# Kernel optimization log

Hardware: AMD Instinct MI355X
Metric: run time of the kernel (lower is better)

Reference implementation:

```python
import jax, jax.numpy as jnp
import numpy as np

H, M, K, V, FF = 16, 1024, 64, 64, 4096
B, C = 2, 2048
EPS = 1e-5


def layer_norm(x, g, b):
    mu = jnp.mean(x, axis=-1, keepdims=True)
    var = jnp.mean(jnp.square(x - mu), axis=-1, keepdims=True)
    return (x - mu) * jax.lax.rsqrt(var + EPS) * g + b


def setup_inputs() -> dict:
    key = jax.random.key(0)
    ks = jax.random.split(key, 7)
    return {
        "x": jax.random.normal(ks[0], (B, C, M), dtype=jnp.float32),
        "wq": jax.random.normal(ks[1], (H, M, K), dtype=jnp.float32),
        "wk": jax.random.normal(ks[2], (H, M, K), dtype=jnp.float32),
        "wv": jax.random.normal(ks[3], (H, M, V), dtype=jnp.float32),
        "wo": jax.random.normal(ks[4], (H, V, M), dtype=jnp.float32),
        "ln1_g": jnp.ones((M,), jnp.float32),
        "ln1_b": jnp.zeros((M,), jnp.float32),
        "w1": jax.random.normal(ks[5], (M, FF), dtype=jnp.float32),
        "b1": jnp.zeros((FF,), jnp.float32),
        "w2": jax.random.normal(ks[6], (FF, M), dtype=jnp.float32),
        "b2": jnp.zeros((M,), jnp.float32),
        "ln2_g": jnp.ones((M,), jnp.float32),
        "ln2_b": jnp.zeros((M,), jnp.float32),
    }


def reference(x, wq, wk, wv, wo, ln1_g, ln1_b, w1, b1, w2, b2, ln2_g, ln2_b):
    # --- multi-head self-attention (kv = q = x) ---
    kval = jnp.einsum('bcm,hmk->bhck', x, wk)
    vval = jnp.einsum('bcm,hmv->bhcv', x, wv)
    qval = jnp.einsum('bdm,hmk->bhdk', x, wq)
    # logits: c indexes keys, d indexes queries; softmax over keys (axis 2)
    logits = jnp.einsum('bhck,bhdk->bhcd', kval, qval) / np.sqrt(K).astype(np.float32)
    att = jax.nn.softmax(logits, axis=2)
    pre = jnp.einsum('bhcd,bhcv->bhdv', att, vval)
    attn_out = jnp.einsum('bhdv,hvm->bdm', pre, wo)
    h1 = layer_norm(x + attn_out, ln1_g, ln1_b)
    # --- position-wise FFN ---
    s = jax.nn.relu(jnp.einsum('bcm,mf->bcf', h1, w1) + b1)
    ffn_out = jnp.einsum('bcf,fm->bcm', s, w2) + b2
    return layer_norm(h1 + ffn_out, ln2_g, ln2_b)
```

## Files before the change

kernel.cpp:

```cpp
#include <hip/hip_runtime.h>
#include <hip/hip_bf16.h>

#define Hn 16
#define Mn 1024
#define FFn 4096
#define Bn 2
#define Cn 2048
#define EPSf 1e-5f
#define MB (1024LL*1024LL)

typedef unsigned short u16;
typedef __attribute__((ext_vector_type(8))) short bf16x8;
typedef __attribute__((ext_vector_type(4))) float f32x4;
typedef __attribute__((ext_vector_type(8))) unsigned short u16x8;

#define MFMA(a,b,c) __builtin_amdgcn_mfma_f32_16x16x32_bf16(a, b, c, 0, 0, 0)

__device__ __forceinline__ u16 f2b(float v) {
    union { float f; unsigned int u; } x; x.f = v;
    unsigned int r = x.u + 0x7fffu + ((x.u >> 16) & 1u);
    return (u16)(r >> 16);
}
__device__ __forceinline__ float b2f(u16 b) {
    union { unsigned int u; float f; } x; x.u = ((unsigned int)b) << 16;
    return x.f;
}
__device__ __forceinline__ void glds16(const void* g, void* l) {
    __builtin_amdgcn_global_load_lds((const __attribute__((address_space(1))) void*)g,
                                     (__attribute__((address_space(3))) void*)l, 16, 0, 0);
}

__global__ __launch_bounds__(256) void split_cvt(const float* __restrict__ in,
    u16* __restrict__ hi, u16* __restrict__ lo)
{
    const long i = ((long)blockIdx.x * 256 + threadIdx.x) * 8;
    float4 a = *(const float4*)&in[i];
    float4 b = *(const float4*)&in[i + 4];
    float v[8] = {a.x,a.y,a.z,a.w,b.x,b.y,b.z,b.w};
    u16x8 h, l;
#pragma unroll
    for (int j = 0; j < 8; ++j) {
        u16 hh = f2b(v[j]);
        h[j] = hh;
        l[j] = f2b(v[j] - b2f(hh));
    }
    *(u16x8*)&hi[i] = h;
    *(u16x8*)&lo[i] = l;
}

template<bool SPLIT>
__global__ __launch_bounds__(256) void tcvt(const float* __restrict__ in,
    u16* __restrict__ outh, u16* __restrict__ outl, int R, int Cc)
{
    __shared__ float ts[64][65];
    const int t = threadIdx.x;
    const long ib = (long)blockIdx.z * R * Cc;
    const int r0 = blockIdx.y * 64, c0 = blockIdx.x * 64;
    const int rr = t >> 2, cb = (t & 3) * 16;
#pragma unroll
    for (int u = 0; u < 4; ++u) {
        float4 v = *(const float4*)&in[ib + (long)(r0 + rr) * Cc + c0 + cb + u * 4];
        ts[rr][cb + u*4 + 0] = v.x; ts[rr][cb + u*4 + 1] = v.y;
        ts[rr][cb + u*4 + 2] = v.z; ts[rr][cb + u*4 + 3] = v.w;
    }
    __syncthreads();
    const int oc = t >> 2;
#pragma unroll
    for (int u = 0; u < 4; ++u) {
        float vv[4];
#pragma unroll
        for (int j = 0; j < 4; ++j) vv[j] = ts[cb + u*4 + j][oc];
        ushort4 hh;
        hh.x = f2b(vv[0]); hh.y = f2b(vv[1]); hh.z = f2b(vv[2]); hh.w = f2b(vv[3]);
        *(ushort4*)&outh[ib + (long)(c0 + oc) * R + r0 + cb + u*4] = hh;
        if (SPLIT) {
            ushort4 ll;
            ll.x = f2b(vv[0] - b2f(hh.x)); ll.y = f2b(vv[1] - b2f(hh.y));
            ll.z = f2b(vv[2] - b2f(hh.z)); ll.w = f2b(vv[3] - b2f(hh.w));
            *(ushort4*)&outl[ib + (long)(c0 + oc) * R + r0 + cb + u*4] = ll;
        }
    }
}

__global__ __launch_bounds__(256) void ttrans(const u16* __restrict__ in,
    u16* __restrict__ out, int R, int Cc)
{
    __shared__ u16 ts[64][72];
    const int t = threadIdx.x;
    const long ib = (long)blockIdx.z * R * Cc;
    const int r0 = blockIdx.y * 64, c0 = blockIdx.x * 64;
    const int rr = t >> 2, cb = (t & 3) * 16;
#pragma unroll
    for (int u = 0; u < 2; ++u)
        *(u16x8*)&ts[rr][cb + u*8] =
            *(const u16x8*)&in[ib + (long)(r0 + rr) * Cc + c0 + cb + u*8];
    __syncthreads();
    const int oc = t >> 2;
#pragma unroll
    for (int u = 0; u < 4; ++u) {
        ushort4 p;
        p.x = ts[cb + u*4 + 0][oc]; p.y = ts[cb + u*4 + 1][oc];
        p.z = ts[cb + u*4 + 2][oc]; p.w = ts[cb + u*4 + 3][oc];
        *(ushort4*)&out[ib + (long)(c0 + oc) * R + r0 + cb + u*4] = p;
    }
}

template<bool OUTB16, bool BIAS, bool RELU>
__global__ __launch_bounds__(256) void gemm128(
    const u16* __restrict__ A, const u16* __restrict__ Bt,
    const float* __restrict__ bias, void* __restrict__ Cout,
    int Kdim, int lda, int ldbt, int ldc)
{
    __shared__ u16 Als[128*32];
    __shared__ u16 Bls[128*32];
    const int t = threadIdx.x, w = t >> 6, l = t & 63;
    const int wm = w >> 1, wn = w & 1;
    const long row0 = (long)blockIdx.y * 128;
    const int n0 = blockIdx.x * 128;
    const int sr = l >> 2, sc = (l & 3) * 8;
    f32x4 acc[4][4] = {};
    for (int k0 = 0; k0 < Kdim; k0 += 32) {
        __syncthreads();
#pragma unroll
        for (int i = 0; i < 2; ++i) {
            const int c = w*2 + i;
            glds16(&A[(row0 + c*16 + sr) * lda + k0 + sc], (char*)Als + c*1024);
            glds16(&Bt[((long)n0 + c*16 + sr) * ldbt + k0 + sc], (char*)Bls + c*1024);
        }
        __syncthreads();
        bf16x8 af[4], bfv[4];
#pragma unroll
        for (int mf = 0; mf < 4; ++mf)
            af[mf] = *(const bf16x8*)&Als[(wm*64 + mf*16 + (l&15))*32 + (l>>4)*8];
#pragma unroll
        for (int nf = 0; nf < 4; ++nf)
            bfv[nf] = *(const bf16x8*)&Bls[(wn*64 + nf*16 + (l&15))*32 + (l>>4)*8];
#pragma unroll
        for (int mf = 0; mf < 4; ++mf)
#pragma unroll
            for (int nf = 0; nf < 4; ++nf)
                acc[mf][nf] = MFMA(af[mf], bfv[nf], acc[mf][nf]);
    }
#pragma unroll
    for (int nf = 0; nf < 4; ++nf) {
        const int col = n0 + wn*64 + nf*16 + (l & 15);
        const float bv = BIAS ? bias[col] : 0.f;
#pragma unroll
        for (int mf = 0; mf < 4; ++mf)
#pragma unroll
            for (int r = 0; r < 4; ++r) {
                const long row = row0 + wm*64 + mf*16 + (l>>4)*4 + r;
                float v = acc[mf][nf][r] + bv;
                if (RELU) v = fmaxf(v, 0.f);
                if (OUTB16) ((u16*)Cout)[row * ldc + col] = f2b(v);
                else        ((float*)Cout)[row * ldc + col] = v;
            }
    }
}

template<bool SIN, bool SOUT>
__global__ __launch_bounds__(256) void gemm64(
    const u16* __restrict__ Ah, const u16* __restrict__ Alo,
    const u16* __restrict__ Bth, const u16* __restrict__ Btl,
    u16* __restrict__ Chi, u16* __restrict__ Clo, float scale,
    int Kdim, int lda, int ldbt,
    int aDiv, long aStride, int bMod, long bStride, long cStride)
{
    extern __shared__ u16 lds[];
    u16* AH = lds;
    u16* BH = lds + 4096;
    u16* AL = lds + 6144;
    u16* BL = lds + 10240;
    const int t = threadIdx.x, w = t >> 6, l = t & 63;
    const int wm = w >> 1, wn = w & 1;
    const int z = blockIdx.z;
    const u16* Ahb = Ah + (long)(z / aDiv) * aStride;
    const u16* Alb = SIN ? (Alo + (long)(z / aDiv) * aStride) : (const u16*)nullptr;
    const u16* Bhb = Bth + (long)(z % bMod) * bStride;
    const u16* Blb = SIN ? (Btl + (long)(z % bMod) * bStride) : (const u16*)nullptr;
    const long row0 = (long)blockIdx.y * 128;
    const int sr = l >> 2, sc = (l & 3) * 8;
    f32x4 acc[4][2] = {};
    const int NCH = SIN ? 6 : 3;
    for (int k0 = 0; k0 < Kdim; k0 += 32) {
        __syncthreads();
        for (int i = 0; i < NCH; ++i) {
            const int idx = w + i*4;
            if (idx < 8)
                glds16(&Ahb[(row0 + idx*16 + sr)*lda + k0 + sc], (char*)AH + idx*1024);
            else if (idx < 12)
                glds16(&Bhb[(long)((idx-8)*16 + sr)*ldbt + k0 + sc], (char*)BH + (idx-8)*1024);
            else if (idx < 20)
                glds16(&Alb[(row0 + (idx-12)*16 + sr)*lda + k0 + sc], (char*)AL + (idx-12)*1024);
            else
                glds16(&Blb[(long)((idx-20)*16 + sr)*ldbt + k0 + sc], (char*)BL + (idx-20)*1024);
        }
        __syncthreads();
        bf16x8 ah[4], bh[2], al[4], bl[2];
#pragma unroll
        for (int mf = 0; mf < 4; ++mf)
            ah[mf] = *(const bf16x8*)&AH[(wm*64 + mf*16 + (l&15))*32 + (l>>4)*8];
#pragma unroll
        for (int nf = 0; nf < 2; ++nf)
            bh[nf] = *(const bf16x8*)&BH[(wn*32 + nf*16 + (l&15))*32 + (l>>4)*8];
        if (SIN) {
#pragma unroll
            for (int mf = 0; mf < 4; ++mf)
                al[mf] = *(const bf16x8*)&AL[(wm*64 + mf*16 + (l&15))*32 + (l>>4)*8];
#pragma unroll
            for (int nf = 0; nf < 2; ++nf)
                bl[nf] = *(const bf16x8*)&BL[(wn*32 + nf*16 + (l&15))*32 + (l>>4)*8];
        }
#pragma unroll
        for (int mf = 0; mf < 4; ++mf)
#pragma unroll
            for (int nf = 0; nf < 2; ++nf) {
                acc[mf][nf] = MFMA(ah[mf], bh[nf], acc[mf][nf]);
                if (SIN) {
                    acc[mf][nf] = MFMA(ah[mf], bl[nf], acc[mf][nf]);
                    acc[mf][nf] = MFMA(al[mf], bh[nf], acc[mf][nf]);
                }
            }
    }
    u16* Cb  = Chi + (long)z * cStride;
    u16* Clb = SOUT ? (Clo + (long)z * cStride) : (u16*)nullptr;
#pragma unroll
    for (int mf = 0; mf < 4; ++mf)
#pragma unroll
        for (int nf = 0; nf < 2; ++nf)
#pragma unroll
            for (int r = 0; r < 4; ++r) {
                const long row = row0 + wm*64 + mf*16 + (l>>4)*4 + r;
                const int col = wn*32 + nf*16 + (l & 15);
                const float v = acc[mf][nf][r] * scale;
                const u16 hh = f2b(v);
                Cb[row*64 + col] = hh;
                if (SOUT) Clb[row*64 + col] = f2b(v - b2f(hh));
            }
}

__global__ __launch_bounds__(256) void attn_mfma(
    const u16* __restrict__ qh, const u16* __restrict__ ql,
    const u16* __restrict__ kh, const u16* __restrict__ kl,
    const u16* __restrict__ vt, u16* __restrict__ pre2b)
{
    __shared__ u16 QH[4096], QL[4096], KH[4096], KL[4096], VT[4096];
    __shared__ u16 PL[4][1152];
    const int t = threadIdx.x, w = t >> 6, l = t & 63;
    const int bh = blockIdx.y, b = bh >> 4, h = bh & 15;
    const int q0 = blockIdx.x * 64;
    const long base = (long)bh * Cn * 64;
    const int srow = l >> 3;
    const int gch  = (l & 7) ^ (l >> 3);

#pragma unroll
    for (int i = 0; i < 2; ++i) {
        const int ci = w*2 + i;
        const int row = ci*8 + srow;
        glds16(&qh[base + (long)(q0 + row)*64 + gch*8], (char*)QH + ci*1024);
        glds16(&ql[base + (long)(q0 + row)*64 + gch*8], (char*)QL + ci*1024);
    }
    __syncthreads();
    bf16x8 qfh[2], qfl[2];
#pragma unroll
    for (int ks = 0; ks < 2; ++ks) {
        const int row = w*16 + (l & 15);
        const int ch = ((l>>4) + ks*4) ^ (row & 7);
        qfh[ks] = *(const bf16x8*)&QH[row*64 + ch*8];
        qfl[ks] = *(const bf16x8*)&QL[row*64 + ch*8];
    }
    float m_[4], ls_[4];
    f32x4 o[4] = {};
#pragma unroll
    for (int r = 0; r < 4; ++r) { m_[r] = -1e30f; ls_[r] = 0.f; }

    for (int c0 = 0; c0 < Cn; c0 += 64) {
        __syncthreads();
#pragma unroll
        for (int i = 0; i < 2; ++i) {
            const int ci = w*2 + i;
            const int row = ci*8 + srow;
            glds16(&kh[base + (long)(c0 + row)*64 + gch*8], (char*)KH + ci*1024);
            glds16(&kl[base + (long)(c0 + row)*64 + gch*8], (char*)KL + ci*1024);
            glds16(&vt[base + (long)row*Cn + c0 + gch*8],   (char*)VT + ci*1024);
        }
        __syncthreads();
        f32x4 sc[4];
#pragma unroll
        for (int cf = 0; cf < 4; ++cf) {
            f32x4 a = {0.f, 0.f, 0.f, 0.f};
#pragma unroll
            for (int ks = 0; ks < 2; ++ks) {
                const int row = cf*16 + (l & 15);
                const int ch = ((l>>4) + ks*4) ^ (row & 7);
                const bf16x8 kfh = *(const bf16x8*)&KH[row*64 + ch*8];
                const bf16x8 kfl = *(const bf16x8*)&KL[row*64 + ch*8];
                a = MFMA(qfh[ks], kfh, a);
                a = MFMA(qfh[ks], kfl, a);
                a = MFMA(qfl[ks], kfh, a);
            }
            sc[cf] = a;
        }
        float mx[4];
#pragma unroll
        for (int r = 0; r < 4; ++r)
            mx[r] = fmaxf(fmaxf(sc[0][r], sc[1][r]), fmaxf(sc[2][r], sc[3][r]));
#pragma unroll
        for (int off = 1; off < 16; off <<= 1)
#pragma unroll
            for (int r = 0; r < 4; ++r)
                mx[r] = fmaxf(mx[r], __shfl_xor(mx[r], off, 64));
        float fct[4], rs_[4];
#pragma unroll
        for (int r = 0; r < 4; ++r) {
            const float mn = fmaxf(m_[r], mx[r]);
            fct[r] = __expf(m_[r] - mn);
            m_[r] = mn;
            rs_[r] = 0.f;
        }
#pragma unroll
        for (int cf = 0; cf < 4; ++cf)
#pragma unroll
            for (int r = 0; r < 4; ++r) {
                const float p = __expf(sc[cf][r] - m_[r]);
                rs_[r] += p;
                PL[w][((l>>4)*4 + r)*72 + cf*16 + (l & 15)] = f2b(p);
            }
#pragma unroll
        for (int off = 1; off < 16; off <<= 1)
#pragma unroll
            for (int r = 0; r < 4; ++r)
                rs_[r] += __shfl_xor(rs_[r], off, 64);
#pragma unroll
        for (int r = 0; r < 4; ++r)
            ls_[r] = ls_[r] * fct[r] + rs_[r];
#pragma unroll
        for (int vf = 0; vf < 4; ++vf)
#pragma unroll
            for (int r = 0; r < 4; ++r)
                o[vf][r] *= fct[r];
        bf16x8 pa[2];
#pragma unroll
        for (int ks = 0; ks < 2; ++ks)
            pa[ks] = *(const bf16x8*)&PL[w][(l&15)*72 + ks*32 + (l>>4)*8];
#pragma unroll
        for (int vf = 0; vf < 4; ++vf)
#pragma unroll
            for (int ks = 0; ks < 2; ++ks) {
                const int row = vf*16 + (l & 15);
                const int ch = ((l>>4) + ks*4) ^ (row & 7);
                const bf16x8 vfr = *(const bf16x8*)&VT[row*64 + ch*8];
                o[vf] = MFMA(pa[ks], vfr, o[vf]);
            }
    }
    float inv[4];
#pragma unroll
    for (int r = 0; r < 4; ++r) inv[r] = 1.f / ls_[r];
#pragma unroll
    for (int vf = 0; vf < 4; ++vf)
#pragma unroll
        for (int r = 0; r < 4; ++r) {
            const long q = q0 + w*16 + (l>>4)*4 + r;
            pre2b[((long)b*Cn + q)*1024 + h*64 + vf*16 + (l&15)] = f2b(o[vf][r] * inv[r]);
        }
}

template<bool WB16>
__global__ __launch_bounds__(256) void ln_res(
    const float* __restrict__ a, const float* __restrict__ r,
    const float* __restrict__ g, const float* __restrict__ be,
    float* __restrict__ out, u16* __restrict__ outb)
{
    __shared__ float wsum[4];
    __shared__ float wsum2[4];
    const long row = blockIdx.x;
    const int t = threadIdx.x;
    float4 va = *(const float4*)&a[row * Mn + t * 4];
    float4 vb = *(const float4*)&r[row * Mn + t * 4];
    float v0 = va.x + vb.x, v1 = va.y + vb.y, v2 = va.z + vb.z, v3 = va.w + vb.w;

    float s = v0 + v1 + v2 + v3;
#pragma unroll
    for (int off = 32; off > 0; off >>= 1) s += __shfl_xor(s, off, 64);
    if ((t & 63) == 0) wsum[t >> 6] = s;
    __syncthreads();
    float mu = (wsum[0] + wsum[1] + wsum[2] + wsum[3]) * (1.0f / Mn);

    float d0 = v0 - mu, d1 = v1 - mu, d2 = v2 - mu, d3 = v3 - mu;
    float s2 = d0 * d0 + d1 * d1 + d2 * d2 + d3 * d3;
#pragma unroll
    for (int off = 32; off > 0; off >>= 1) s2 += __shfl_xor(s2, off, 64);
    if ((t & 63) == 0) wsum2[t >> 6] = s2;
    __syncthreads();
    float var = (wsum2[0] + wsum2[1] + wsum2[2] + wsum2[3]) * (1.0f / Mn);
    float rstd = rsqrtf(var + EPSf);

    float4 g4 = *(const float4*)&g[t * 4];
    float4 b4 = *(const float4*)&be[t * 4];
    float4 r4;
    r4.x = d0 * rstd * g4.x + b4.x;
    r4.y = d1 * rstd * g4.y + b4.y;
    r4.z = d2 * rstd * g4.z + b4.z;
    r4.w = d3 * rstd * g4.w + b4.w;
    *(float4*)&out[row * Mn + t * 4] = r4;
    if (WB16) {
        ushort4 ob;
        ob.x = f2b(r4.x); ob.y = f2b(r4.y); ob.z = f2b(r4.z); ob.w = f2b(r4.w);
        *(ushort4*)&outb[row * Mn + t * 4] = ob;
    }
}

extern "C" void kernel_launch(void* const* d_in, const int* in_sizes, int n_in,
                              void* d_out, int out_size, void* d_ws, size_t ws_size,
                              hipStream_t stream)
{
    const float* x    = (const float*)d_in[0];
    const float* wq   = (const float*)d_in[1];
    const float* wk   = (const float*)d_in[2];
    const float* wv   = (const float*)d_in[3];
    const float* wo   = (const float*)d_in[4];
    const float* ln1g = (const float*)d_in[5];
    const float* ln1b = (const float*)d_in[6];
    const float* w1   = (const float*)d_in[7];
    const float* b1   = (const float*)d_in[8];
    const float* w2   = (const float*)d_in[9];
    const float* b2   = (const float*)d_in[10];
    const float* ln2g = (const float*)d_in[11];
    const float* ln2b = (const float*)d_in[12];
    float* out = (float*)d_out;

    char* W = (char*)d_ws;
    u16* x_hi  = (u16*)(W + 0*MB);
    u16* x_lo  = (u16*)(W + 8*MB);
    u16* wqTh  = (u16*)(W + 16*MB);
    u16* wqTl  = (u16*)(W + 18*MB);
    u16* wkTh  = (u16*)(W + 20*MB);
    u16* wkTl  = (u16*)(W + 22*MB);
    u16* wvT   = (u16*)(W + 24*MB);
    u16* woT   = (u16*)(W + 26*MB);
    u16* q_hi  = (u16*)(W + 28*MB);
    u16* q_lo  = (u16*)(W + 36*MB);
    u16* k_hi  = (u16*)(W + 44*MB);
    u16* k_lo  = (u16*)(W + 52*MB);
    u16* vb    = (u16*)(W + 60*MB);
    u16* vTb   = (u16*)(W + 68*MB);
    u16* pre2b = (u16*)(W + 76*MB);
    float* attn_tmp = (float*)(W + 28*MB);
    float* h1  = (float*)(W + 44*MB);
    u16* h1b   = (u16*)(W + 60*MB);
    u16* w1T   = (u16*)(W + 68*MB);
    u16* w2T   = (u16*)(W + 76*MB);
    u16* sbuf  = (u16*)(W + 0*MB);
    float* ffn = (float*)(W + 60*MB);

    const long CM = (long)Cn * Mn;
    const long WS = 64LL * 1024;
    const long CS = (long)Cn * 64;

    split_cvt<<<2048, 256, 0, stream>>>(x, x_hi, x_lo);
    tcvt<true ><<<dim3(1,16,16), 256, 0, stream>>>(wq, wqTh, wqTl, 1024, 64);
    tcvt<true ><<<dim3(1,16,16), 256, 0, stream>>>(wk, wkTh, wkTl, 1024, 64);
    tcvt<false><<<dim3(1,16,16), 256, 0, stream>>>(wv, wvT, nullptr, 1024, 64);
    tcvt<false><<<dim3(16,16,1), 256, 0, stream>>>(wo, woT, nullptr, 1024, 1024);

    gemm64<true,true ><<<dim3(1,16,32), 256, 24576, stream>>>(
        x_hi, x_lo, wqTh, wqTl, q_hi, q_lo, 0.125f, 1024, 1024, 1024, 16, CM, 16, WS, CS);
    gemm64<true,true ><<<dim3(1,16,32), 256, 24576, stream>>>(
        x_hi, x_lo, wkTh, wkTl, k_hi, k_lo, 1.0f,   1024, 1024, 1024, 16, CM, 16, WS, CS);
    gemm64<false,false><<<dim3(1,16,32), 256, 12288, stream>>>(
        x_hi, nullptr, wvT, nullptr, vb, nullptr, 1.0f, 1024, 1024, 1024, 16, CM, 16, WS, CS);
    ttrans<<<dim3(1,32,32), 256, 0, stream>>>(vb, vTb, 2048, 64);

    attn_mfma<<<dim3(32,32), 256, 0, stream>>>(q_hi, q_lo, k_hi, k_lo, vTb, pre2b);

    tcvt<false><<<dim3(64,16,1), 256, 0, stream>>>(w1, w1T, nullptr, 1024, 4096);

    gemm128<false,false,false><<<dim3(8,32), 256, 0, stream>>>(
        pre2b, woT, nullptr, attn_tmp, 1024, 1024, 1024, 1024);
    tcvt<false><<<dim3(16,64,1), 256, 0, stream>>>(w2, w2T, nullptr, 4096, 1024);

    ln_res<true ><<<Bn*Cn, 256, 0, stream>>>(x, attn_tmp, ln1g, ln1b, h1, h1b);

    gemm128<true,true,true ><<<dim3(32,32), 256, 0, stream>>>(
        h1b, w1T, b1, sbuf, 1024, 1024, 1024, 4096);

    gemm128<false,true,false><<<dim3(8,32), 256, 0, stream>>>(
        sbuf, w2T, b2, ffn, 4096, 4096, 4096, 1024);

    ln_res<false><<<Bn*Cn, 256, 0, stream>>>(h1, ffn, ln2g, ln2b, out, nullptr);
}
```

Baseline: 583.1 us.

## Fuse Q and K projections into one wide split-precision GEMM

Replaces the per-head gemm64 projections with the 128x128 gemm128 kernel, which now optionally takes hi/lo split-bf16 inputs and outputs. Q and K weights are concatenated so one GEMM writes a [B*C, 2048] QK buffer, with per-column scaling applying 1/8 to the Q half. The V projection becomes a single flat GEMM, and the transpose and attention kernels read the head-interleaved layout directly. The aim is fewer launches and larger tiles that reuse x across all heads, at the cost of more LDS per block and strided head access in attention.

```diff
diff --git a/kernel.cpp b/kernel.cpp
--- a/kernel.cpp
+++ b/kernel.cpp
@@ -82,18 +82,18 @@
     }
 }
 
-__global__ __launch_bounds__(256) void ttrans(const u16* __restrict__ in,
-    u16* __restrict__ out, int R, int Cc)
+__global__ __launch_bounds__(256) void ttrans2(const u16* __restrict__ in,
+    u16* __restrict__ out)
 {
     __shared__ u16 ts[64][72];
     const int t = threadIdx.x;
-    const long ib = (long)blockIdx.z * R * Cc;
-    const int r0 = blockIdx.y * 64, c0 = blockIdx.x * 64;
+    const int bh = blockIdx.z, b = bh >> 4, h = bh & 15;
+    const int c0 = blockIdx.x * 64;
     const int rr = t >> 2, cb = (t & 3) * 16;
 #pragma unroll
     for (int u = 0; u < 2; ++u)
         *(u16x8*)&ts[rr][cb + u*8] =
-            *(const u16x8*)&in[ib + (long)(r0 + rr) * Cc + c0 + cb + u*8];
+            *(const u16x8*)&in[((long)b*Cn + c0 + rr) * 1024 + h*64 + cb + u*8];
     __syncthreads();
     const int oc = t >> 2;
 #pragma unroll
@@ -101,155 +101,108 @@
         ushort4 p;
         p.x = ts[cb + u*4 + 0][oc]; p.y = ts[cb + u*4 + 1][oc];
         p.z = ts[cb + u*4 + 2][oc]; p.w = ts[cb + u*4 + 3][oc];
-        *(ushort4*)&out[ib + (long)(c0 + oc) * R + r0 + cb + u*4] = p;
-    }
-}
-
-template<bool OUTB16, bool BIAS, bool RELU>
+        *(ushort4*)&out[(long)bh*64*Cn + (long)oc*Cn + c0 + cb + u*4] = p;
+    }
+}
+
+template<bool SIN, bool SOUT, bool OUTB16, bool BIAS, bool RELU>
 __global__ __launch_bounds__(256) void gemm128(
-    const u16* __restrict__ A, const u16* __restrict__ Bt,
+    const u16* __restrict__ A, const u16* __restrict__ Al,
+    const u16* __restrict__ Bt, const u16* __restrict__ Btl,
     const float* __restrict__ bias, void* __restrict__ Cout,
+    u16* __restrict__ Clo, float s1, float s2, int scol,
     int Kdim, int lda, int ldbt, int ldc)
 {
-    __shared__ u16 Als[128*32];
-    __shared__ u16 Bls[128*32];
+    __shared__ u16 lds[SIN ? 16384 : 8192];
     const int t = threadIdx.x, w = t >> 6, l = t & 63;
     const int wm = w >> 1, wn = w & 1;
     const long row0 = (long)blockIdx.y * 128;
     const int n0 = blockIdx.x * 128;
     const int sr = l >> 2, sc = (l & 3) * 8;
     f32x4 acc[4][4] = {};
+    const int NCH = SIN ? 8 : 4;
     for (int k0 = 0; k0 < Kdim; k0 += 32) {
         __syncthreads();
 #pragma unroll
-        for (int i = 0; i < 2; ++i) {
-            const int c = w*2 + i;
-            glds16(&A[(row0 + c*16 + sr) * lda + k0 + sc], (char*)Als + c*1024);
-            glds16(&Bt[((long)n0 + c*16 + sr) * ldbt + k0 + sc], (char*)Bls + c*1024);
-        }
-        __syncthreads();
-        bf16x8 af[4], bfv[4];
-#pragma unroll
-        for (int mf = 0; mf < 4; ++mf)
-            af[mf] = *(const bf16x8*)&Als[(wm*64 + mf*16 + (l&15))*32 + (l>>4)*8];
-#pragma unroll
-        for (int nf = 0; nf < 4; ++nf)
-            bfv[nf] = *(const bf16x8*)&Bls[(wn*64 + nf*16 + (l&15))*32 + (l>>4)*8];
-#pragma unroll
-        for (int mf = 0; mf < 4; ++mf)
-#pragma unroll
-            for (int nf = 0; nf < 4; ++nf)
-                acc[mf][nf] = MFMA(af[mf], bfv[nf], acc[mf][nf]);
-    }
-#pragma unroll
-    for (int nf = 0; nf < 4; ++nf) {
-        const int col = n0 + wn*64 + nf*16 + (l & 15);
-        const float bv = BIAS ? bias[col] : 0.f;
-#pragma unroll
-        for (int mf = 0; mf < 4; ++mf)
-#pragma unroll
-            for (int r = 0; r < 4; ++r) {
-                const long row = row0 + wm*64 + mf*16 + (l>>4)*4 + r;
-                float v = acc[mf][nf][r] + bv;
-                if (RELU) v = fmaxf(v, 0.f);
-                if (OUTB16) ((u16*)Cout)[row * ldc + col] = f2b(v);
-                else        ((float*)Cout)[row * ldc + col] = v;
-            }
-    }
-}
-
-template<bool SIN, bool SOUT>
-__global__ __launch_bounds__(256) void gemm64(
-    const u16* __restrict__ Ah, const u16* __restrict__ Alo,
-    const u16* __restrict__ Bth, const u16* __restrict__ Btl,
-    u16* __restrict__ Chi, u16* __restrict__ Clo, float scale,
-    int Kdim, int lda, int ldbt,
-    int aDiv, long aStride, int bMod, long bStride, long cStride)
-{
-    extern __shared__ u16 lds[];
-    u16* AH = lds;
-    u16* BH = lds + 4096;
-    u16* AL = lds + 6144;
-    u16* BL = lds + 10240;
-    const int t = threadIdx.x, w = t >> 6, l = t & 63;
-    const int wm = w >> 1, wn = w & 1;
-    const int z = blockIdx.z;
-    const u16* Ahb = Ah + (long)(z / aDiv) * aStride;
-    const u16* Alb = SIN ? (Alo + (long)(z / aDiv) * aStride) : (const u16*)nullptr;
-    const u16* Bhb = Bth + (long)(z % bMod) * bStride;
-    const u16* Blb = SIN ? (Btl + (long)(z % bMod) * bStride) : (const u16*)nullptr;
-    const long row0 = (long)blockIdx.y * 128;
-    const int sr = l >> 2, sc = (l & 3) * 8;
-    f32x4 acc[4][2] = {};
-    const int NCH = SIN ? 6 : 3;
-    for (int k0 = 0; k0 < Kdim; k0 += 32) {
-        __syncthreads();
         for (int i = 0; i < NCH; ++i) {
             const int idx = w + i*4;
             if (idx < 8)
-                glds16(&Ahb[(row0 + idx*16 + sr)*lda + k0 + sc], (char*)AH + idx*1024);
-            else if (idx < 12)
-                glds16(&Bhb[(long)((idx-8)*16 + sr)*ldbt + k0 + sc], (char*)BH + (idx-8)*1024);
-            else if (idx < 20)
-                glds16(&Alb[(row0 + (idx-12)*16 + sr)*lda + k0 + sc], (char*)AL + (idx-12)*1024);
+                glds16(&A[(row0 + idx*16 + sr)*lda + k0 + sc], (char*)lds + idx*1024);
+            else if (idx < 16)
+                glds16(&Bt[((long)n0 + (idx-8)*16 + sr)*ldbt + k0 + sc], (char*)lds + 8192 + (idx-8)*1024);
+            else if (idx < 24)
+                glds16(&Al[(row0 + (idx-16)*16 + sr)*lda + k0 + sc], (char*)lds + 16384 + (idx-16)*1024);
             else
-                glds16(&Blb[(long)((idx-20)*16 + sr)*ldbt + k0 + sc], (char*)BL + (idx-20)*1024);
+                glds16(&Btl[((long)n0 + (idx-24)*16 + sr)*ldbt + k0 + sc], (char*)lds + 24576 + (idx-24)*1024);
         }
         __syncthreads();
-        bf16x8 ah[4], bh[2], al[4], bl[2];
+        bf16x8 af[4], bfv[4], alf[4], blf[4];
 #pragma unroll
         for (int mf = 0; mf < 4; ++mf)
-            ah[mf] = *(const bf16x8*)&AH[(wm*64 + mf*16 + (l&15))*32 + (l>>4)*8];
-#pragma unroll
-        for (int nf = 0; nf < 2; ++nf)
-            bh[nf] = *(const bf16x8*)&BH[(wn*32 + nf*16 + (l&15))*32 + (l>>4)*8];
+            af[mf] = *(const bf16x8*)&lds[(wm*64 + mf*16 + (l&15))*32 + (l>>4)*8];
+#pragma unroll
+        for (int nf = 0; nf < 4; ++nf)
+            bfv[nf] = *(const bf16x8*)&lds[4096 + (wn*64 + nf*16 + (l&15))*32 + (l>>4)*8];
         if (SIN) {
 #pragma unroll
             for (int mf = 0; mf < 4; ++mf)
-                al[mf] = *(const bf16x8*)&AL[(wm*64 + mf*16 + (l&15))*32 + (l>>4)*8];
-#pragma unroll
-            for (int nf = 0; nf < 2; ++nf)
-                bl[nf] = *(const bf16x8*)&BL[(wn*32 + nf*16 + (l&15))*32 + (l>>4)*8];
+                alf[mf] = *(const bf16x8*)&lds[8192 + (wm*64 + mf*16 + (l&15))*32 + (l>>4)*8];
+#pragma unroll
+            for (int nf = 0; nf < 4; ++nf)
+                blf[nf] = *(const bf16x8*)&lds[12288 + (wn*64 + nf*16 + (l&15))*32 + (l>>4)*8];
         }
 #pragma unroll
         for (int mf = 0; mf < 4; ++mf)
 #pragma unroll
-            for (int nf = 0; nf < 2; ++nf) {
-                acc[mf][nf] = MFMA(ah[mf], bh[nf], acc[mf][nf]);
+            for (int nf = 0; nf < 4; ++nf) {
+                acc[mf][nf] = MFMA(af[mf], bfv[nf], acc[mf][nf]);
                 if (SIN) {
-                    acc[mf][nf] = MFMA(ah[mf], bl[nf], acc[mf][nf]);
-                    acc[mf][nf] = MFMA(al[mf], bh[nf], acc[mf][nf]);
+                    acc[mf][nf] = MFMA(af[mf], blf[nf], acc[mf][nf]);
+                    acc[mf][nf] = MFMA(alf[mf], bfv[nf], acc[mf][nf]);
                 }
             }
     }
-    u16* Cb  = Chi + (long)z * cStride;
-    u16* Clb = SOUT ? (Clo + (long)z * cStride) : (u16*)nullptr;
-#pragma unroll
-    for (int mf = 0; mf < 4; ++mf)
-#pragma unroll
-        for (int nf = 0; nf < 2; ++nf)
+#pragma unroll
+    for (int nf = 0; nf < 4; ++nf) {
+        const int col = n0 + wn*64 + nf*16 + (l & 15);
+        const float scf = (col < scol) ? s1 : s2;
+        const float bv = BIAS ? bias[col] : 0.f;
+#pragma unroll
+        for (int mf = 0; mf < 4; ++mf)
 #pragma unroll
             for (int r = 0; r < 4; ++r) {
                 const long row = row0 + wm*64 + mf*16 + (l>>4)*4 + r;
-                const int col = wn*32 + nf*16 + (l & 15);
-                const float v = acc[mf][nf][r] * scale;
-                const u16 hh = f2b(v);
-                Cb[row*64 + col] = hh;
-                if (SOUT) Clb[row*64 + col] = f2b(v - b2f(hh));
+                float v = acc[mf][nf][r] * scf + bv;
+                if (RELU) v = fmaxf(v, 0.f);
+                if (OUTB16) {
+                    const u16 hh = f2b(v);
+                    ((u16*)Cout)[row * ldc + col] = hh;
+                    if (SOUT) Clo[row * ldc + col] = f2b(v - b2f(hh));
+                } else {
+                    ((float*)Cout)[row * ldc + col] = v;
+                }
             }
+    }
 }
 
 __global__ __launch_bounds__(256) void attn_mfma(
-    const u16* __restrict__ qh, const u16* __restrict__ ql,
-    const u16* __restrict__ kh, const u16* __restrict__ kl,
+    const u16* __restrict__ qkh, const u16* __restrict__ qkl,
     const u16* __restrict__ vt, u16* __restrict__ pre2b)
 {
-    __shared__ u16 QH[4096], QL[4096], KH[4096], KL[4096], VT[4096];
-    __shared__ u16 PL[4][1152];
+    __shared__ u16 SH[20480];
+    u16* KH = SH;
+    u16* KL = SH + 4096;
+    u16* VT = SH + 8192;
+    u16* QH = SH + 12288;
+    u16* QL = SH + 16384;
+    u16* PL = SH + 12288;
+
     const int t = threadIdx.x, w = t >> 6, l = t & 63;
     const int bh = blockIdx.y, b = bh >> 4, h = bh & 15;
     const int q0 = blockIdx.x * 64;
-    const long base = (long)bh * Cn * 64;
+    const long rbase = (long)b * Cn;
+    const int hoff = h * 64;
+    const long vbase = (long)bh * 64 * Cn;
     const int srow = l >> 3;
     const int gch  = (l & 7) ^ (l >> 3);
 
@@ -257,8 +210,8 @@
     for (int i = 0; i < 2; ++i) {
         const int ci = w*2 + i;
         const int row = ci*8 + srow;
-        glds16(&qh[base + (long)(q0 + row)*64 + gch*8], (char*)QH + ci*1024);
-        glds16(&ql[base + (long)(q0 + row)*64 + gch*8], (char*)QL + ci*1024);
+        glds16(&qkh[(rbase + q0 + row)*2048 + hoff + gch*8], (char*)QH + ci*1024);
+        glds16(&qkl[(rbase + q0 + row)*2048 + hoff + gch*8], (char*)QL + ci*1024);
     }
     __syncthreads();
     bf16x8 qfh[2], qfl[2];
@@ -280,12 +233,12 @@
         for (int i = 0; i < 2; ++i) {
             const int ci = w*2 + i;
             const int row = ci*8 + srow;
-            glds16(&kh[base + (long)(c0 + row)*64 + gch*8], (char*)KH + ci*1024);
-            glds16(&kl[base + (long)(c0 + row)*64 + gch*8], (char*)KL + ci*1024);
-            glds16(&vt[base + (long)row*Cn + c0 + gch*8],   (char*)VT + ci*1024);
+            glds16(&qkh[(rbase + c0 + row)*2048 + 1024 + hoff + gch*8], (char*)KH + ci*1024);
+            glds16(&qkl[(rbase + c0 + row)*2048 + 1024 + hoff + gch*8], (char*)KL + ci*1024);
+            glds16(&vt[vbase + (long)row*Cn + c0 + gch*8], (char*)VT + ci*1024);
         }
         __syncthreads();
-        f32x4 sc[4];
+        f32x4 scv[4];
 #pragma unroll
         for (int cf = 0; cf < 4; ++cf) {
             f32x4 a = {0.f, 0.f, 0.f, 0.f};
@@ -299,12 +252,12 @@
                 a = MFMA(qfh[ks], kfl, a);
                 a = MFMA(qfl[ks], kfh, a);
             }
-            sc[cf] = a;
+            scv[cf] = a;
         }
         float mx[4];
 #pragma unroll
         for (int r = 0; r < 4; ++r)
-            mx[r] = fmaxf(fmaxf(sc[0][r], sc[1][r]), fmaxf(sc[2][r], sc[3][r]));
+            mx[r] = fmaxf(fmaxf(scv[0][r], scv[1][r]), fmaxf(scv[2][r], scv[3][r]));
 #pragma unroll
         for (int off = 1; off < 16; off <<= 1)
 #pragma unroll
@@ -322,9 +275,9 @@
         for (int cf = 0; cf < 4; ++cf)
 #pragma unroll
             for (int r = 0; r < 4; ++r) {
-                const float p = __expf(sc[cf][r] - m_[r]);
+                const float p = __expf(scv[cf][r] - m_[r]);
                 rs_[r] += p;
-                PL[w][((l>>4)*4 + r)*72 + cf*16 + (l & 15)] = f2b(p);
+                PL[w*1152 + ((l>>4)*4 + r)*72 + cf*16 + (l & 15)] = f2b(p);
             }
 #pragma unroll
         for (int off = 1; off < 16; off <<= 1)
@@ -342,7 +295,7 @@
         bf16x8 pa[2];
 #pragma unroll
         for (int ks = 0; ks < 2; ++ks)
-            pa[ks] = *(const bf16x8*)&PL[w][(l&15)*72 + ks*32 + (l>>4)*8];
+            pa[ks] = *(const bf16x8*)&PL[w*1152 + (l&15)*72 + ks*32 + (l>>4)*8];
 #pragma unroll
         for (int vf = 0; vf < 4; ++vf)
 #pragma unroll
@@ -432,16 +385,12 @@
     char* W = (char*)d_ws;
     u16* x_hi  = (u16*)(W + 0*MB);
     u16* x_lo  = (u16*)(W + 8*MB);
-    u16* wqTh  = (u16*)(W + 16*MB);
-    u16* wqTl  = (u16*)(W + 18*MB);
-    u16* wkTh  = (u16*)(W + 20*MB);
-    u16* wkTl  = (u16*)(W + 22*MB);
+    u16* wqkTh = (u16*)(W + 16*MB);
+    u16* wqkTl = (u16*)(W + 20*MB);
     u16* wvT   = (u16*)(W + 24*MB);
     u16* woT   = (u16*)(W + 26*MB);
-    u16* q_hi  = (u16*)(W + 28*MB);
-    u16* q_lo  = (u16*)(W + 36*MB);
-    u16* k_hi  = (u16*)(W + 44*MB);
-    u16* k_lo  = (u16*)(W + 52*MB);
+    u16* qk_hi = (u16*)(W + 28*MB);
+    u16* qk_lo = (u16*)(W + 44*MB);
     u16* vb    = (u16*)(W + 60*MB);
     u16* vTb   = (u16*)(W + 68*MB);
     u16* pre2b = (u16*)(W + 76*MB);
@@ -453,39 +402,38 @@
     u16* sbuf  = (u16*)(W + 0*MB);
     float* ffn = (float*)(W + 60*MB);
 
-    const long CM = (long)Cn * Mn;
-    const long WS = 64LL * 1024;
-    const long CS = (long)Cn * 64;
-
     split_cvt<<<2048, 256, 0, stream>>>(x, x_hi, x_lo);
-    tcvt<true ><<<dim3(1,16,16), 256, 0, stream>>>(wq, wqTh, wqTl, 1024, 64);
-    tcvt<true ><<<dim3(1,16,16), 256, 0, stream>>>(wk, wkTh, wkTl, 1024, 64);
+    tcvt<true ><<<dim3(1,16,16), 256, 0, stream>>>(wq, wqkTh, wqkTl, 1024, 64);
+    tcvt<true ><<<dim3(1,16,16), 256, 0, stream>>>(wk, wqkTh + 1048576, wqkTl + 1048576, 1024, 64);
     tcvt<false><<<dim3(1,16,16), 256, 0, stream>>>(wv, wvT, nullptr, 1024, 64);
     tcvt<false><<<dim3(16,16,1), 256, 0, stream>>>(wo, woT, nullptr, 1024, 1024);
 
-    gemm64<true,true ><<<dim3(1,16,32), 256, 24576, stream>>>(
-        x_hi, x_lo, wqTh, wqTl, q_hi, q_lo, 0.125f, 1024, 1024, 1024, 16, CM, 16, WS, CS);
-    gemm64<true,true ><<<dim3(1,16,32), 256, 24576, stream>>>(
-        x_hi, x_lo, wkTh, wkTl, k_hi, k_lo, 1.0f,   1024, 1024, 1024, 16, CM, 16, WS, CS);
-    gemm64<false,false><<<dim3(1,16,32), 256, 12288, stream>>>(
-        x_hi, nullptr, wvT, nullptr, vb, nullptr, 1.0f, 1024, 1024, 1024, 16, CM, 16, WS, CS);
-    ttrans<<<dim3(1,32,32), 256, 0, stream>>>(vb, vTb, 2048, 64);
-
-    attn_mfma<<<dim3(32,32), 256, 0, stream>>>(q_hi, q_lo, k_hi, k_lo, vTb, pre2b);
+    gemm128<true,true,true,false,false><<<dim3(16,32), 256, 0, stream>>>(
+        x_hi, x_lo, wqkTh, wqkTl, nullptr, qk_hi, qk_lo,
+        0.125f, 1.0f, 1024, 1024, 1024, 1024, 2048);
+    gemm128<false,false,true,false,false><<<dim3(8,32), 256, 0, stream>>>(
+        x_hi, nullptr, wvT, nullptr, nullptr, vb, nullptr,
+        1.f, 1.f, 0, 1024, 1024, 1024, 1024);
+    ttrans2<<<dim3(32,1,32), 256, 0, stream>>>(vb, vTb);
+
+    attn_mfma<<<dim3(32,32), 256, 0, stream>>>(qk_hi, qk_lo, vTb, pre2b);
 
     tcvt<false><<<dim3(64,16,1), 256, 0, stream>>>(w1, w1T, nullptr, 1024, 4096);
 
-    gemm128<false,false,false><<<dim3(8,32), 256, 0, stream>>>(
-        pre2b, woT, nullptr, attn_tmp, 1024, 1024, 1024, 1024);
+    gemm128<false,false,false,false,false><<<dim3(8,32), 256, 0, stream>>>(
+        pre2b, nullptr, woT, nullptr, nullptr, attn_tmp, nullptr,
+        1.f, 1.f, 0, 1024, 1024, 1024, 1024);
     tcvt<false><<<dim3(16,64,1), 256, 0, stream>>>(w2, w2T, nullptr, 4096, 1024);
 
     ln_res<true ><<<Bn*Cn, 256, 0, stream>>>(x, attn_tmp, ln1g, ln1b, h1, h1b);
 
-    gemm128<true,true,true ><<<dim3(32,32), 256, 0, stream>>>(
-        h1b, w1T, b1, sbuf, 1024, 1024, 1024, 4096);
-
-    gemm128<false,true,false><<<dim3(8,32), 256, 0, stream>>>(
-        sbuf, w2T, b2, ffn, 4096, 4096, 4096, 1024);
+    gemm128<false,false,true,true,true ><<<dim3(32,32), 256, 0, stream>>>(
+        h1b, nullptr, w1T, nullptr, b1, sbuf, nullptr,
+        1.f, 1.f, 0, 1024, 1024, 1024, 4096);
+
+    gemm128<false,false,false,true,false><<<dim3(8,32), 256, 0, stream>>>(
+        sbuf, nullptr, w2T, nullptr, b2, ffn, nullptr,
+        1.f, 1.f, 0, 4096, 4096, 4096, 1024);
 
     ln_res<false><<<Bn*Cn, 256, 0, stream>>>(h1, ffn, ln2g, ln2b, out, nullptr);
 }
```

After: 550.7 us. 5.6% less time.
